# Optimization experiments

Hardware: AMD Instinct MI355X
Metric: run time of the kernel (lower is better)

## Reference

```python
import jax, jax.numpy as jnp
import numpy as np

DIM = 1024
NUM_HEADS = 16
HEAD_DIM = DIM // NUM_HEADS
SCALE = HEAD_DIM ** -0.5


def setup_inputs() -> dict:
    key = jax.random.key(0)
    ks = jax.random.split(key, 6)
    B, N = 2, 2048
    s = DIM ** -0.5
    return {
        "x": jax.random.normal(ks[0], (B, N, DIM), dtype=jnp.float32),
        "Wq": jax.random.normal(ks[1], (DIM, DIM), dtype=jnp.float32) * s,
        "Wk": jax.random.normal(ks[2], (DIM, DIM), dtype=jnp.float32) * s,
        "Wv": jax.random.normal(ks[3], (DIM, DIM), dtype=jnp.float32) * s,
        "Wp": jax.random.normal(ks[4], (DIM, DIM), dtype=jnp.float32) * s,
        "bp": jax.random.normal(ks[5], (DIM,), dtype=jnp.float32) * 0.01,
    }


def reference(x, Wq, Wk, Wv, Wp, bp):
    B, N, C = x.shape
    H, D = NUM_HEADS, HEAD_DIM
    # projections (torch Linear: x @ W.T); reshape to (B, H, N, D)
    q = (x @ Wq.T).reshape(B, N, H, D).transpose(0, 2, 1, 3)
    k = (x @ Wk.T).reshape(B, N, H, D).transpose(0, 2, 1, 3)
    v = (x @ Wv.T).reshape(B, N, H, D).transpose(0, 2, 1, 3)
    attn = jnp.einsum("bhnd,bhmd->bhnm", q, k) * SCALE
    attn = jax.nn.softmax(attn, axis=-1)  # dropout p=0 -> identity
    out = jnp.einsum("bhnm,bhmd->bhnd", attn, v)
    out = out.transpose(0, 2, 1, 3).reshape(B, N, C)
    return out @ Wp.T + bp
```

## Files before the change

### kernel.cpp

```cpp
#include <hip/hip_runtime.h>
#include <cstdint>

#define DIMC   1024
#define NHEADS 16
#define HD     64
#define BATCH  2
#define SEQ    2048
#define MROWS  (BATCH*SEQ)
#define QSCALE2 0.18033688f

typedef __bf16 bf16x8 __attribute__((ext_vector_type(8)));
typedef float  f32x4  __attribute__((ext_vector_type(4)));

#define AST 88
#define TST 136

__device__ __forceinline__ unsigned short f2bf(float f) {
    union { float f; unsigned int u; } v; v.f = f;
    unsigned int u = v.u;
    u += 0x7fffu + ((u >> 16) & 1u);
    return (unsigned short)(u >> 16);
}

__device__ __forceinline__ unsigned int pk2bf(float a, float b) {
    union { float f; unsigned int u; } ua, ub;
    ua.f = a; ub.f = b;
    return __builtin_amdgcn_perm(ub.u + 0x8000u, ua.u + 0x8000u, 0x07060302u);
}

__device__ __forceinline__ void gload_lds16(const void* g, void* l) {
    __builtin_amdgcn_global_load_lds(
        (const __attribute__((address_space(1))) unsigned int*)g,
        (__attribute__((address_space(3))) unsigned int*)l, 16, 0, 0);
}

__global__ __launch_bounds__(256) void cast_all(
    const float* __restrict__ x,
    const float* __restrict__ Wq, const float* __restrict__ Wk,
    const float* __restrict__ Wv, const float* __restrict__ Wp,
    unsigned short* __restrict__ xb, unsigned short* __restrict__ Wb)
{
    const size_t M1 = (size_t)DIMC * DIMC;
    int y = blockIdx.y;
    const float* src;
    unsigned short* dst;
    if (y < 4)      { src = x  + (size_t)y * M1; dst = xb + (size_t)y * M1; }
    else if (y == 4){ src = Wq; dst = Wb; }
    else if (y == 5){ src = Wk; dst = Wb + M1; }
    else if (y == 6){ src = Wv; dst = Wb + 2 * M1; }
    else            { src = Wp; dst = Wb + 3 * M1; }
    size_t idx = ((size_t)blockIdx.x * 256 + threadIdx.x) * 4;
    float4 v = *(const float4*)(src + idx);
    ushort4 p; p.x = f2bf(v.x); p.y = f2bf(v.y); p.z = f2bf(v.z); p.w = f2bf(v.w);
    *(ushort4*)(dst + idx) = p;
}

__device__ __forceinline__ void gemm_issue(
    const unsigned short* __restrict__ A, const unsigned short* __restrict__ B,
    unsigned short* As, unsigned short* Bs, int m0, int n0, int kt)
{
    const int t = threadIdx.x;
    const int w = t >> 6, lane = t & 63;
    const int srow = lane >> 3, scol = lane & 7;
#pragma unroll
    for (int i = 0; i < 4; ++i) {
        int r  = i * 32 + w * 8 + srow;
        int cg = scol ^ (r & 7);
        gload_lds16(A + (size_t)(m0 + r) * DIMC + kt + cg * 8, As + r * 64 + scol * 8);
        gload_lds16(B + (size_t)(n0 + r) * DIMC + kt + cg * 8, Bs + r * 64 + scol * 8);
    }
}

__device__ __forceinline__ void gemm_compute(
    const unsigned short* As, const unsigned short* Bs, f32x4 acc[4][4])
{
    const int t = threadIdx.x;
    const int w = t >> 6, lane = t & 63, quad = lane >> 4, lr = lane & 15;
    const int wr = w >> 1, wc = w & 1;
#pragma unroll
    for (int kk = 0; kk < 2; ++kk) {
        bf16x8 af[4], bfr[4];
#pragma unroll
        for (int mt = 0; mt < 4; ++mt) {
            int row = wr * 64 + mt * 16 + lr;
            int cb  = kk * 4 + quad;
            af[mt] = *(const bf16x8*)&As[row * 64 + (cb ^ (row & 7)) * 8];
        }
#pragma unroll
        for (int nt = 0; nt < 4; ++nt) {
            int row = wc * 64 + nt * 16 + lr;
            int cb  = kk * 4 + quad;
            bfr[nt] = *(const bf16x8*)&Bs[row * 64 + (cb ^ (row & 7)) * 8];
        }
#pragma unroll
        for (int mt = 0; mt < 4; ++mt)
#pragma unroll
            for (int nt = 0; nt < 4; ++nt)
                acc[mt][nt] = __builtin_amdgcn_mfma_f32_16x16x32_bf16(af[mt], bfr[nt], acc[mt][nt], 0, 0, 0);
    }
}

__device__ __forceinline__ void gemm_k_loop_db(
    const unsigned short* __restrict__ A, const unsigned short* __restrict__ B,
    unsigned short* smem, int m0, int n0, f32x4 acc[4][4])
{
    unsigned short* As0 = smem;
    unsigned short* Bs0 = smem + 8192;
    unsigned short* As1 = smem + 16384;
    unsigned short* Bs1 = smem + 24576;

    gemm_issue(A, B, As0, Bs0, m0, n0, 0);
    for (int kt = 0; kt < DIMC; kt += 128) {
        __syncthreads();
        gemm_issue(A, B, As1, Bs1, m0, n0, kt + 64);
        gemm_compute(As0, Bs0, acc);
        __syncthreads();
        if (kt + 128 < DIMC) gemm_issue(A, B, As0, Bs0, m0, n0, kt + 128);
        gemm_compute(As1, Bs1, acc);
    }
}

__device__ __forceinline__ void vt_epilogue(
    unsigned short* Ts, f32x4 acc[4][4], int m0, int n0,
    unsigned short* __restrict__ vT)
{
    const int t = threadIdx.x;
    const int w = t >> 6, lane = t & 63, quad = lane >> 4, lr = lane & 15;
    const int wr = w >> 1, wc = w & 1;

    __syncthreads();
#pragma unroll
    for (int mt = 0; mt < 4; ++mt)
#pragma unroll
        for (int nt = 0; nt < 4; ++nt) {
            int lcol  = wc * 64 + nt * 16 + lr;
            int lrow0 = wr * 64 + mt * 16 + quad * 4;
            ushort4 p;
            p.x = f2bf(acc[mt][nt][0]); p.y = f2bf(acc[mt][nt][1]);
            p.z = f2bf(acc[mt][nt][2]); p.w = f2bf(acc[mt][nt][3]);
            *(ushort4*)&Ts[lcol * TST + lrow0] = p;
        }
    __syncthreads();

    int lc = t >> 1, half = t & 1;
    int cg = n0 + lc, hh = cg >> 6, dd = cg & 63;
    int bb = m0 >> 11, nn0 = m0 & (SEQ - 1);
    size_t dst = ((size_t)((bb * NHEADS + hh) * HD + dd)) * SEQ + nn0 + half * 64;
    const unsigned short* srcp = &Ts[lc * TST + half * 64];
#pragma unroll
    for (int i = 0; i < 8; ++i)
        *(uint4*)&vT[dst + i * 8] = *(const uint4*)&srcp[i * 8];
}

__global__ __launch_bounds__(256) void gemm_qkv_fast(
    const unsigned short* __restrict__ xb, const unsigned short* __restrict__ Wb,
    unsigned short* __restrict__ qo, unsigned short* __restrict__ ko,
    unsigned short* __restrict__ vT)
{
    __shared__ unsigned short smem[32768];

    const int t  = threadIdx.x;
    const int n0 = blockIdx.x * 128, m0 = blockIdx.y * 128, z = blockIdx.z;
    const unsigned short* B = Wb + (size_t)z * DIMC * DIMC;
    const int w = t >> 6, lane = t & 63, quad = lane >> 4, lr = lane & 15;
    const int wr = w >> 1, wc = w & 1;

    f32x4 acc[4][4];
#pragma unroll
    for (int mt = 0; mt < 4; ++mt)
#pragma unroll
        for (int nt = 0; nt < 4; ++nt)
#pragma unroll
            for (int r = 0; r < 4; ++r) acc[mt][nt][r] = 0.f;

    gemm_k_loop_db(xb, B, smem, m0, n0, acc);

    if (z == 2) {
        vt_epilogue(smem, acc, m0, n0, vT);
    } else {
        unsigned short* Out = (z == 0) ? qo : ko;
        const float sc = (z == 0) ? QSCALE2 : 1.0f;
#pragma unroll
        for (int mt = 0; mt < 4; ++mt)
#pragma unroll
            for (int nt = 0; nt < 4; ++nt)
#pragma unroll
                for (int r = 0; r < 4; ++r) {
                    int row = m0 + wr * 64 + mt * 16 + quad * 4 + r;
                    int col = n0 + wc * 64 + nt * 16 + lr;
                    Out[(size_t)row * DIMC + col] = f2bf(acc[mt][nt][r] * sc);
                }
    }
}

__global__ __launch_bounds__(256) void gemm_out_fast(
    const unsigned short* __restrict__ O, const unsigned short* __restrict__ Wpb,
    const float* __restrict__ bias, float* __restrict__ out)
{
    __shared__ unsigned short smem[32768];

    const int t  = threadIdx.x;
    const int n0 = blockIdx.x * 128, m0 = blockIdx.y * 128;
    const int w = t >> 6, lane = t & 63, quad = lane >> 4, lr = lane & 15;
    const int wr = w >> 1, wc = w & 1;

    f32x4 acc[4][4];
#pragma unroll
    for (int mt = 0; mt < 4; ++mt)
#pragma unroll
        for (int nt = 0; nt < 4; ++nt)
#pragma unroll
            for (int r = 0; r < 4; ++r) acc[mt][nt][r] = 0.f;

    gemm_k_loop_db(O, Wpb, smem, m0, n0, acc);

#pragma unroll
    for (int mt = 0; mt < 4; ++mt)
#pragma unroll
        for (int nt = 0; nt < 4; ++nt)
#pragma unroll
            for (int r = 0; r < 4; ++r) {
                int row = m0 + wr * 64 + mt * 16 + quad * 4 + r;
                int col = n0 + wc * 64 + nt * 16 + lr;
                out[(size_t)row * DIMC + col] = acc[mt][nt][r] + bias[col];
            }
}

__global__ __launch_bounds__(256) void attn_kernel(
    const unsigned short* __restrict__ qg, const unsigned short* __restrict__ kg,
    const unsigned short* __restrict__ vT, unsigned short* __restrict__ og)
{
    __shared__ unsigned short Ka[64 * 64];
    __shared__ unsigned short Kb[64 * 64];
    __shared__ unsigned short Va[64 * 64];
    __shared__ unsigned short Vb[64 * 64];
    __shared__ unsigned short Ps[128 * 64];

    const int t  = threadIdx.x;
    const int w = t >> 6, l = t & 63, quad = l >> 4, lr = l & 15;
    const int srow = t >> 3, scol = t & 7;
    const int pkey = (lr & 7) << 1;

    const int bid  = blockIdx.x;
    const int slot = bid >> 3;
    const int bh   = (bid & 7) * 4 + (slot >> 4);
    const int qt   = slot & 15;
    const int b    = bh >> 4, h = bh & 15;

    const unsigned short* khead = kg + ((size_t)(b * SEQ)) * DIMC + h * HD;
    const unsigned short* vhead = vT + (size_t)((b * NHEADS + h) * HD) * SEQ;

    bf16x8 qf[2][2];
#pragma unroll
    for (int mt = 0; mt < 2; ++mt) {
        const size_t qoff = ((size_t)(b * SEQ + qt * 128 + w * 32 + mt * 16 + lr)) * DIMC + h * HD;
        qf[mt][0] = *(const bf16x8*)(qg + qoff + 0  + quad * 8);
        qf[mt][1] = *(const bf16x8*)(qg + qoff + 32 + quad * 8);
    }

    bf16x8 ones;
#pragma unroll
    for (int j = 0; j < 8; ++j) ones[j] = (__bf16)1.0f;
    const f32x4 fzero = { 0.f, 0.f, 0.f, 0.f };

    f32x4 o_acc[2][4], lacc[2];
#pragma unroll
    for (int mt = 0; mt < 2; ++mt) {
        lacc[mt] = fzero;
#pragma unroll
        for (int ct = 0; ct < 4; ++ct) o_acc[mt][ct] = fzero;
    }

    auto issue = [&](int kt, unsigned short* Kd, unsigned short* Vd) {
#pragma unroll
        for (int i = 0; i < 2; ++i) {
            int r  = i * 32 + srow;
            int cg = scol ^ (r & 7);
            gload_lds16(khead + (size_t)(kt * 64 + r) * DIMC + cg * 8, Kd + r * 64 + scol * 8);
            gload_lds16(vhead + (size_t)r * SEQ + kt * 64 + cg * 8,   Vd + r * 64 + scol * 8);
        }
    };

    auto compute = [&](const unsigned short* Kc, const unsigned short* Vc) {
        f32x4 s[2][4];
#pragma unroll
        for (int nt = 0; nt < 4; ++nt) {
            int row = nt * 16 + lr;
            bf16x8 kf = *(const bf16x8*)&Kc[row * 64 + ((quad ^ (row & 7)) * 8)];
#pragma unroll
            for (int mt = 0; mt < 2; ++mt)
                s[mt][nt] = __builtin_amdgcn_mfma_f32_16x16x32_bf16(kf, qf[mt][0], fzero, 0, 0, 0);
        }
#pragma unroll
        for (int nt = 0; nt < 4; ++nt) {
            int row = nt * 16 + lr;
            bf16x8 kf = *(const bf16x8*)&Kc[row * 64 + (((4 + quad) ^ (row & 7)) * 8)];
#pragma unroll
            for (int mt = 0; mt < 2; ++mt)
                s[mt][nt] = __builtin_amdgcn_mfma_f32_16x16x32_bf16(kf, qf[mt][1], s[mt][nt], 0, 0, 0);
        }

#pragma unroll
        for (int mt = 0; mt < 2; ++mt)
#pragma unroll
            for (int nt = 0; nt < 4; ++nt) {
                uint2 pp;
                pp.x = pk2bf(__builtin_amdgcn_exp2f(s[mt][nt][0]),
                             __builtin_amdgcn_exp2f(s[mt][nt][1]));
                pp.y = pk2bf(__builtin_amdgcn_exp2f(s[mt][nt][2]),
                             __builtin_amdgcn_exp2f(s[mt][nt][3]));
                *(uint2*)&Ps[(w * 32 + mt * 16 + lr) * 64 + (((nt * 4 + quad) ^ pkey) * 4)] = pp;
            }

#pragma unroll
        for (int kk = 0; kk < 2; ++kk) {
            bf16x8 vf[4];
#pragma unroll
            for (int ct = 0; ct < 4; ++ct) {
                int row = ct * 16 + lr;
                vf[ct] = *(const bf16x8*)&Vc[row * 64 + (((kk * 4 + quad) ^ (row & 7)) * 8)];
            }
#pragma unroll
            for (int mt = 0; mt < 2; ++mt) {
                bf16x8 pf = *(const bf16x8*)&Ps[(w * 32 + mt * 16 + lr) * 64 + (((kk * 8 + quad * 2) ^ pkey) * 4)];
                lacc[mt] = __builtin_amdgcn_mfma_f32_16x16x32_bf16(pf, ones, lacc[mt], 0, 0, 0);
#pragma unroll
                for (int ct = 0; ct < 4; ++ct)
                    o_acc[mt][ct] = __builtin_amdgcn_mfma_f32_16x16x32_bf16(pf, vf[ct], o_acc[mt][ct], 0, 0, 0);
            }
        }
    };

    issue(0, Ka, Va);
    for (int kt = 0; kt < SEQ / 64; kt += 2) {
        __syncthreads();
        issue(kt + 1, Kb, Vb);
        compute(Ka, Va);

        __syncthreads();
        if (kt + 2 < SEQ / 64) issue(kt + 2, Ka, Va);
        compute(Kb, Vb);
    }

#pragma unroll
    for (int mt = 0; mt < 2; ++mt) {
        float inv[4];
#pragma unroll
        for (int r = 0; r < 4; ++r) inv[r] = 1.0f / lacc[mt][r];
#pragma unroll
        for (int ct = 0; ct < 4; ++ct)
#pragma unroll
            for (int r = 0; r < 4; ++r) {
                int qrow = qt * 128 + w * 32 + mt * 16 + quad * 4 + r;
                og[((size_t)(b * SEQ + qrow)) * DIMC + h * HD + ct * 16 + lr] =
                    f2bf(o_acc[mt][ct][r] * inv[r]);
            }
    }
}

__global__ __launch_bounds__(256) void gemm_qkv_f32(
    const float* __restrict__ x,
    const float* __restrict__ Wq, const float* __restrict__ Wk, const float* __restrict__ Wv,
    unsigned short* __restrict__ qo, unsigned short* __restrict__ ko, unsigned short* __restrict__ vT)
{
    __shared__ unsigned short smem[2 * 128 * AST];
    unsigned short* As = smem;
    unsigned short* Bs = smem + 128 * AST;

    const int t  = threadIdx.x;
    const int n0 = blockIdx.x * 128, m0 = blockIdx.y * 128, z = blockIdx.z;
    const float* W = (z == 0) ? Wq : (z == 1) ? Wk : Wv;
    const int w = t >> 6, l = t & 63, quad = l >> 4, lr = l & 15;
    const int wr = w >> 1, wc = w & 1;

    f32x4 acc[4][4];
#pragma unroll
    for (int mt = 0; mt < 4; ++mt)
#pragma unroll
        for (int nt = 0; nt < 4; ++nt)
#pragma unroll
            for (int r = 0; r < 4; ++r) acc[mt][nt][r] = 0.f;

    for (int kt = 0; kt < DIMC; kt += 64) {
        __syncthreads();
#pragma unroll
        for (int i = 0; i < 8; ++i) {
            int flat = t + i * 256;
            int row = flat >> 4, seg = flat & 15;
            float4 a = *(const float4*)(x + (size_t)(m0 + row) * DIMC + kt + seg * 4);
            ushort4 pa; pa.x = f2bf(a.x); pa.y = f2bf(a.y); pa.z = f2bf(a.z); pa.w = f2bf(a.w);
            *(ushort4*)&As[row * AST + seg * 4] = pa;
            float4 b = *(const float4*)(W + (size_t)(n0 + row) * DIMC + kt + seg * 4);
            ushort4 pb; pb.x = f2bf(b.x); pb.y = f2bf(b.y); pb.z = f2bf(b.z); pb.w = f2bf(b.w);
            *(ushort4*)&Bs[row * AST + seg * 4] = pb;
        }
        __syncthreads();
#pragma unroll
        for (int kk = 0; kk < 2; ++kk) {
            bf16x8 af[4], bfr[4];
#pragma unroll
            for (int mt = 0; mt < 4; ++mt)
                af[mt] = *(const bf16x8*)&As[(wr * 64 + mt * 16 + lr) * AST + kk * 32 + quad * 8];
#pragma unroll
            for (int nt = 0; nt < 4; ++nt)
                bfr[nt] = *(const bf16x8*)&Bs[(wc * 64 + nt * 16 + lr) * AST + kk * 32 + quad * 8];
#pragma unroll
            for (int mt = 0; mt < 4; ++mt)
#pragma unroll
                for (int nt = 0; nt < 4; ++nt)
                    acc[mt][nt] = __builtin_amdgcn_mfma_f32_16x16x32_bf16(af[mt], bfr[nt], acc[mt][nt], 0, 0, 0);
        }
    }

    if (z == 2) {
        __syncthreads();
#pragma unroll
        for (int mt = 0; mt < 4; ++mt)
#pragma unroll
            for (int nt = 0; nt < 4; ++nt) {
                int lcol  = wc * 64 + nt * 16 + lr;
                int lrow0 = wr * 64 + mt * 16 + quad * 4;
                ushort4 p;
                p.x = f2bf(acc[mt][nt][0]); p.y = f2bf(acc[mt][nt][1]);
                p.z = f2bf(acc[mt][nt][2]); p.w = f2bf(acc[mt][nt][3]);
                *(ushort4*)&smem[lcol * TST + lrow0] = p;
            }
        __syncthreads();
        int lc = t >> 1, half = t & 1;
        int cg = n0 + lc, hh = cg >> 6, dd = cg & 63;
        int bb = m0 >> 11, nn0 = m0 & (SEQ - 1);
        size_t dst = ((size_t)((bb * NHEADS + hh) * HD + dd)) * SEQ + nn0 + half * 64;
        const unsigned short* srcp = &smem[lc * TST + half * 64];
#pragma unroll
        for (int i = 0; i < 8; ++i)
            *(uint4*)&vT[dst + i * 8] = *(const uint4*)&srcp[i * 8];
    } else {
        unsigned short* Out = (z == 0) ? qo : ko;
        const float sc = (z == 0) ? QSCALE2 : 1.0f;
#pragma unroll
        for (int mt = 0; mt < 4; ++mt)
#pragma unroll
            for (int nt = 0; nt < 4; ++nt)
#pragma unroll
                for (int r = 0; r < 4; ++r) {
                    int row = m0 + wr * 64 + mt * 16 + quad * 4 + r;
                    int col = n0 + wc * 64 + nt * 16 + lr;
                    Out[(size_t)row * DIMC + col] = f2bf(acc[mt][nt][r] * sc);
                }
    }
}

__global__ __launch_bounds__(256) void gemm_out_f32(
    const unsigned short* __restrict__ A, const float* __restrict__ Wp,
    const float* __restrict__ bias, float* __restrict__ out)
{
    __shared__ unsigned short As[128 * AST];
    __shared__ unsigned short Bs[128 * AST];

    const int t  = threadIdx.x;
    const int n0 = blockIdx.x * 128, m0 = blockIdx.y * 128;
    const int w = t >> 6, l = t & 63, quad = l >> 4, lr = l & 15;
    const int wr = w >> 1, wc = w & 1;

    f32x4 acc[4][4];
#pragma unroll
    for (int mt = 0; mt < 4; ++mt)
#pragma unroll
        for (int nt = 0; nt < 4; ++nt)
#pragma unroll
            for (int r = 0; r < 4; ++r) acc[mt][nt][r] = 0.f;

    for (int kt = 0; kt < DIMC; kt += 64) {
        __syncthreads();
#pragma unroll
        for (int i = 0; i < 8; ++i) {
            int flat = t + i * 256;
            int row = flat >> 4, seg = flat & 15;
            ushort4 a = *(const ushort4*)(A + (size_t)(m0 + row) * DIMC + kt + seg * 4);
            *(ushort4*)&As[row * AST + seg * 4] = a;
            float4 b = *(const float4*)(Wp + (size_t)(n0 + row) * DIMC + kt + seg * 4);
            ushort4 pb; pb.x = f2bf(b.x); pb.y = f2bf(b.y); pb.z = f2bf(b.z); pb.w = f2bf(b.w);
            *(ushort4*)&Bs[row * AST + seg * 4] = pb;
        }
        __syncthreads();
#pragma unroll
        for (int kk = 0; kk < 2; ++kk) {
            bf16x8 af[4], bfr[4];
#pragma unroll
            for (int mt = 0; mt < 4; ++mt)
                af[mt] = *(const bf16x8*)&As[(wr * 64 + mt * 16 + lr) * AST + kk * 32 + quad * 8];
#pragma unroll
            for (int nt = 0; nt < 4; ++nt)
                bfr[nt] = *(const bf16x8*)&Bs[(wc * 64 + nt * 16 + lr) * AST + kk * 32 + quad * 8];
#pragma unroll
            for (int mt = 0; mt < 4; ++mt)
#pragma unroll
                for (int nt = 0; nt < 4; ++nt)
                    acc[mt][nt] = __builtin_amdgcn_mfma_f32_16x16x32_bf16(af[mt], bfr[nt], acc[mt][nt], 0, 0, 0);
        }
    }

#pragma unroll
    for (int mt = 0; mt < 4; ++mt)
#pragma unroll
        for (int nt = 0; nt < 4; ++nt)
#pragma unroll
            for (int r = 0; r < 4; ++r) {
                int row = m0 + wr * 64 + mt * 16 + quad * 4 + r;
                int col = n0 + wc * 64 + nt * 16 + lr;
                out[(size_t)row * DIMC + col] = acc[mt][nt][r] + bias[col];
            }
}

extern "C" void kernel_launch(void* const* d_in, const int* in_sizes, int n_in,
                              void* d_out, int out_size, void* d_ws, size_t ws_size,
                              hipStream_t stream)
{
    const float* x  = (const float*)d_in[0];
    const float* Wq = (const float*)d_in[1];
    const float* Wk = (const float*)d_in[2];
    const float* Wv = (const float*)d_in[3];
    const float* Wp = (const float*)d_in[4];
    const float* bp = (const float*)d_in[5];
    float* out = (float*)d_out;

    const size_t SZ  = (size_t)MROWS * DIMC;
    const size_t WSZ = (size_t)DIMC * DIMC;
    const size_t need = (4 * SZ + 4 * WSZ) * sizeof(unsigned short);

    if (ws_size >= need) {
        unsigned short* q  = (unsigned short*)d_ws;
        unsigned short* k  = q + SZ;
        unsigned short* vt = k + SZ;
        unsigned short* o  = vt + SZ;
        unsigned short* Wb = o + SZ;
        unsigned short* xb = (unsigned short*)d_out;

        cast_all<<<dim3(1024, 8), 256, 0, stream>>>(x, Wq, Wk, Wv, Wp, xb, Wb);
        gemm_qkv_fast<<<dim3(DIMC / 128, MROWS / 128, 3), 256, 0, stream>>>(xb, Wb, q, k, vt);
        attn_kernel<<<dim3(512), 256, 0, stream>>>(q, k, vt, o);
        gemm_out_fast<<<dim3(DIMC / 128, MROWS / 128), 256, 0, stream>>>(o, Wb + 3 * WSZ, bp, out);
    } else {
        unsigned short* q  = (unsigned short*)d_ws;
        unsigned short* k  = q + SZ;
        unsigned short* vt = k + SZ;
        unsigned short* o  = vt + SZ;

        gemm_qkv_f32<<<dim3(DIMC / 128, MROWS / 128, 3), 256, 0, stream>>>(x, Wq, Wk, Wv, q, k, vt);
        attn_kernel<<<dim3(512), 256, 0, stream>>>(q, k, vt, o);
        gemm_out_f32<<<dim3(DIMC / 128, MROWS / 128), 256, 0, stream>>>(o, Wp, bp, out);
    }
}
```

Measured before the change: 179.8 us.

## Split attention over key halves with combine pass; shrink GEMM K-tile to 32

Attention is split into two halves along the key sequence. This doubles the block count from 512 to 1024 to improve occupancy on the many-CU device. Each half writes fp32 partial outputs and row sums, and a new combine kernel merges them into bf16. The QKV and output GEMMs now use a 32-wide K tile, which halves LDS use per block so more blocks can be resident. The V-transpose epilogue gets an XOR-swizzled LDS layout. The costs are extra fp32 traffic for the partial results, one more kernel launch, and more barriers in the GEMM loop.

```diff
diff --git a/kernel.cpp b/kernel.cpp
--- a/kernel.cpp
+++ b/kernel.cpp
@@ -55,72 +55,66 @@
     *(ushort4*)(dst + idx) = p;
 }
 
-__device__ __forceinline__ void gemm_issue(
+__device__ __forceinline__ void gemm_issue32(
     const unsigned short* __restrict__ A, const unsigned short* __restrict__ B,
     unsigned short* As, unsigned short* Bs, int m0, int n0, int kt)
 {
     const int t = threadIdx.x;
-    const int w = t >> 6, lane = t & 63;
-    const int srow = lane >> 3, scol = lane & 7;
-#pragma unroll
-    for (int i = 0; i < 4; ++i) {
-        int r  = i * 32 + w * 8 + srow;
-        int cg = scol ^ (r & 7);
-        gload_lds16(A + (size_t)(m0 + r) * DIMC + kt + cg * 8, As + r * 64 + scol * 8);
-        gload_lds16(B + (size_t)(n0 + r) * DIMC + kt + cg * 8, Bs + r * 64 + scol * 8);
-    }
-}
-
-__device__ __forceinline__ void gemm_compute(
+    const int srow = t >> 2, scol = t & 3;
+#pragma unroll
+    for (int i = 0; i < 2; ++i) {
+        int r  = i * 64 + srow;
+        int cg = scol ^ (r & 3);
+        gload_lds16(A + (size_t)(m0 + r) * DIMC + kt + cg * 8, As + r * 32 + scol * 8);
+        gload_lds16(B + (size_t)(n0 + r) * DIMC + kt + cg * 8, Bs + r * 32 + scol * 8);
+    }
+}
+
+__device__ __forceinline__ void gemm_compute32(
     const unsigned short* As, const unsigned short* Bs, f32x4 acc[4][4])
 {
     const int t = threadIdx.x;
     const int w = t >> 6, lane = t & 63, quad = lane >> 4, lr = lane & 15;
     const int wr = w >> 1, wc = w & 1;
-#pragma unroll
-    for (int kk = 0; kk < 2; ++kk) {
-        bf16x8 af[4], bfr[4];
-#pragma unroll
-        for (int mt = 0; mt < 4; ++mt) {
-            int row = wr * 64 + mt * 16 + lr;
-            int cb  = kk * 4 + quad;
-            af[mt] = *(const bf16x8*)&As[row * 64 + (cb ^ (row & 7)) * 8];
-        }
-#pragma unroll
-        for (int nt = 0; nt < 4; ++nt) {
-            int row = wc * 64 + nt * 16 + lr;
-            int cb  = kk * 4 + quad;
-            bfr[nt] = *(const bf16x8*)&Bs[row * 64 + (cb ^ (row & 7)) * 8];
-        }
-#pragma unroll
-        for (int mt = 0; mt < 4; ++mt)
-#pragma unroll
-            for (int nt = 0; nt < 4; ++nt)
-                acc[mt][nt] = __builtin_amdgcn_mfma_f32_16x16x32_bf16(af[mt], bfr[nt], acc[mt][nt], 0, 0, 0);
-    }
-}
-
-__device__ __forceinline__ void gemm_k_loop_db(
+    bf16x8 af[4], bfr[4];
+#pragma unroll
+    for (int mt = 0; mt < 4; ++mt) {
+        int row = wr * 64 + mt * 16 + lr;
+        af[mt] = *(const bf16x8*)&As[row * 32 + ((quad ^ (row & 3)) * 8)];
+    }
+#pragma unroll
+    for (int nt = 0; nt < 4; ++nt) {
+        int row = wc * 64 + nt * 16 + lr;
+        bfr[nt] = *(const bf16x8*)&Bs[row * 32 + ((quad ^ (row & 3)) * 8)];
+    }
+#pragma unroll
+    for (int mt = 0; mt < 4; ++mt)
+#pragma unroll
+        for (int nt = 0; nt < 4; ++nt)
+            acc[mt][nt] = __builtin_amdgcn_mfma_f32_16x16x32_bf16(af[mt], bfr[nt], acc[mt][nt], 0, 0, 0);
+}
+
+__device__ __forceinline__ void gemm_k_loop32(
     const unsigned short* __restrict__ A, const unsigned short* __restrict__ B,
     unsigned short* smem, int m0, int n0, f32x4 acc[4][4])
 {
     unsigned short* As0 = smem;
-    unsigned short* Bs0 = smem + 8192;
-    unsigned short* As1 = smem + 16384;
-    unsigned short* Bs1 = smem + 24576;
-
-    gemm_issue(A, B, As0, Bs0, m0, n0, 0);
-    for (int kt = 0; kt < DIMC; kt += 128) {
-        __syncthreads();
-        gemm_issue(A, B, As1, Bs1, m0, n0, kt + 64);
-        gemm_compute(As0, Bs0, acc);
-        __syncthreads();
-        if (kt + 128 < DIMC) gemm_issue(A, B, As0, Bs0, m0, n0, kt + 128);
-        gemm_compute(As1, Bs1, acc);
-    }
-}
-
-__device__ __forceinline__ void vt_epilogue(
+    unsigned short* Bs0 = smem + 4096;
+    unsigned short* As1 = smem + 8192;
+    unsigned short* Bs1 = smem + 12288;
+
+    gemm_issue32(A, B, As0, Bs0, m0, n0, 0);
+    for (int kt = 0; kt < DIMC; kt += 64) {
+        __syncthreads();
+        gemm_issue32(A, B, As1, Bs1, m0, n0, kt + 32);
+        gemm_compute32(As0, Bs0, acc);
+        __syncthreads();
+        if (kt + 64 < DIMC) gemm_issue32(A, B, As0, Bs0, m0, n0, kt + 64);
+        gemm_compute32(As1, Bs1, acc);
+    }
+}
+
+__device__ __forceinline__ void vt_epilogue32(
     unsigned short* Ts, f32x4 acc[4][4], int m0, int n0,
     unsigned short* __restrict__ vT)
 {
@@ -135,10 +129,11 @@
         for (int nt = 0; nt < 4; ++nt) {
             int lcol  = wc * 64 + nt * 16 + lr;
             int lrow0 = wr * 64 + mt * 16 + quad * 4;
+            int c = (lrow0 >> 3) ^ (lcol & 7);
             ushort4 p;
             p.x = f2bf(acc[mt][nt][0]); p.y = f2bf(acc[mt][nt][1]);
             p.z = f2bf(acc[mt][nt][2]); p.w = f2bf(acc[mt][nt][3]);
-            *(ushort4*)&Ts[lcol * TST + lrow0] = p;
+            *(ushort4*)&Ts[lcol * 128 + c * 8 + (lrow0 & 7)] = p;
         }
     __syncthreads();
 
@@ -146,10 +141,11 @@
     int cg = n0 + lc, hh = cg >> 6, dd = cg & 63;
     int bb = m0 >> 11, nn0 = m0 & (SEQ - 1);
     size_t dst = ((size_t)((bb * NHEADS + hh) * HD + dd)) * SEQ + nn0 + half * 64;
-    const unsigned short* srcp = &Ts[lc * TST + half * 64];
-#pragma unroll
-    for (int i = 0; i < 8; ++i)
-        *(uint4*)&vT[dst + i * 8] = *(const uint4*)&srcp[i * 8];
+#pragma unroll
+    for (int i = 0; i < 8; ++i) {
+        int c = (half * 8 + i) ^ (lc & 7);
+        *(uint4*)&vT[dst + i * 8] = *(const uint4*)&Ts[lc * 128 + c * 8];
+    }
 }
 
 __global__ __launch_bounds__(256) void gemm_qkv_fast(
@@ -157,7 +153,7 @@
     unsigned short* __restrict__ qo, unsigned short* __restrict__ ko,
     unsigned short* __restrict__ vT)
 {
-    __shared__ unsigned short smem[32768];
+    __shared__ unsigned short smem[16384];
 
     const int t  = threadIdx.x;
     const int n0 = blockIdx.x * 128, m0 = blockIdx.y * 128, z = blockIdx.z;
@@ -173,10 +169,10 @@
 #pragma unroll
             for (int r = 0; r < 4; ++r) acc[mt][nt][r] = 0.f;
 
-    gemm_k_loop_db(xb, B, smem, m0, n0, acc);
+    gemm_k_loop32(xb, B, smem, m0, n0, acc);
 
     if (z == 2) {
-        vt_epilogue(smem, acc, m0, n0, vT);
+        vt_epilogue32(smem, acc, m0, n0, vT);
     } else {
         unsigned short* Out = (z == 0) ? qo : ko;
         const float sc = (z == 0) ? QSCALE2 : 1.0f;
@@ -197,7 +193,7 @@
     const unsigned short* __restrict__ O, const unsigned short* __restrict__ Wpb,
     const float* __restrict__ bias, float* __restrict__ out)
 {
-    __shared__ unsigned short smem[32768];
+    __shared__ unsigned short smem[16384];
 
     const int t  = threadIdx.x;
     const int n0 = blockIdx.x * 128, m0 = blockIdx.y * 128;
@@ -212,7 +208,7 @@
 #pragma unroll
             for (int r = 0; r < 4; ++r) acc[mt][nt][r] = 0.f;
 
-    gemm_k_loop_db(O, Wpb, smem, m0, n0, acc);
+    gemm_k_loop32(O, Wpb, smem, m0, n0, acc);
 
 #pragma unroll
     for (int mt = 0; mt < 4; ++mt)
@@ -336,7 +332,6 @@
         __syncthreads();
         issue(kt + 1, Kb, Vb);
         compute(Ka, Va);
-
         __syncthreads();
         if (kt + 2 < SEQ / 64) issue(kt + 2, Ka, Va);
         compute(Kb, Vb);
@@ -356,6 +351,166 @@
                     f2bf(o_acc[mt][ct][r] * inv[r]);
             }
     }
+}
+
+__global__ __launch_bounds__(256) void attn_split(
+    const unsigned short* __restrict__ qg, const unsigned short* __restrict__ kg,
+    const unsigned short* __restrict__ vT,
+    float* __restrict__ Opart, float* __restrict__ Lpart)
+{
+    __shared__ unsigned short Ka[64 * 64];
+    __shared__ unsigned short Kb[64 * 64];
+    __shared__ unsigned short Va[64 * 64];
+    __shared__ unsigned short Vb[64 * 64];
+    __shared__ unsigned short Ps[128 * 64];
+
+    const int t  = threadIdx.x;
+    const int w = t >> 6, l = t & 63, quad = l >> 4, lr = l & 15;
+    const int srow = t >> 3, scol = t & 7;
+    const int pkey = (lr & 7) << 1;
+
+    const int bid  = blockIdx.x;
+    const int slot = bid >> 3;
+    const int bh   = (bid & 7) * 4 + (slot >> 5);
+    const int rem  = slot & 31;
+    const int qt   = rem >> 1;
+    const int hk   = rem & 1;
+    const int b    = bh >> 4, h = bh & 15;
+    const int kts  = hk * (SEQ / 128);
+
+    float* Op = Opart + (size_t)hk * MROWS * DIMC;
+    float* Lp = Lpart + (size_t)hk * MROWS * NHEADS;
+
+    const unsigned short* khead = kg + ((size_t)(b * SEQ)) * DIMC + h * HD;
+    const unsigned short* vhead = vT + (size_t)((b * NHEADS + h) * HD) * SEQ;
+
+    bf16x8 qf[2][2];
+#pragma unroll
+    for (int mt = 0; mt < 2; ++mt) {
+        const size_t qoff = ((size_t)(b * SEQ + qt * 128 + w * 32 + mt * 16 + lr)) * DIMC + h * HD;
+        qf[mt][0] = *(const bf16x8*)(qg + qoff + 0  + quad * 8);
+        qf[mt][1] = *(const bf16x8*)(qg + qoff + 32 + quad * 8);
+    }
+
+    bf16x8 ones;
+#pragma unroll
+    for (int j = 0; j < 8; ++j) ones[j] = (__bf16)1.0f;
+    const f32x4 fzero = { 0.f, 0.f, 0.f, 0.f };
+
+    f32x4 o_acc[2][4], lacc[2];
+#pragma unroll
+    for (int mt = 0; mt < 2; ++mt) {
+        lacc[mt] = fzero;
+#pragma unroll
+        for (int ct = 0; ct < 4; ++ct) o_acc[mt][ct] = fzero;
+    }
+
+    auto issue = [&](int kt, unsigned short* Kd, unsigned short* Vd) {
+#pragma unroll
+        for (int i = 0; i < 2; ++i) {
+            int r  = i * 32 + srow;
+            int cg = scol ^ (r & 7);
+            gload_lds16(khead + (size_t)(kt * 64 + r) * DIMC + cg * 8, Kd + r * 64 + scol * 8);
+            gload_lds16(vhead + (size_t)r * SEQ + kt * 64 + cg * 8,   Vd + r * 64 + scol * 8);
+        }
+    };
+
+    auto compute = [&](const unsigned short* Kc, const unsigned short* Vc) {
+        f32x4 s[2][4];
+#pragma unroll
+        for (int nt = 0; nt < 4; ++nt) {
+            int row = nt * 16 + lr;
+            bf16x8 kf = *(const bf16x8*)&Kc[row * 64 + ((quad ^ (row & 7)) * 8)];
+#pragma unroll
+            for (int mt = 0; mt < 2; ++mt)
+                s[mt][nt] = __builtin_amdgcn_mfma_f32_16x16x32_bf16(kf, qf[mt][0], fzero, 0, 0, 0);
+        }
+#pragma unroll
+        for (int nt = 0; nt < 4; ++nt) {
+            int row = nt * 16 + lr;
+            bf16x8 kf = *(const bf16x8*)&Kc[row * 64 + (((4 + quad) ^ (row & 7)) * 8)];
+#pragma unroll
+            for (int mt = 0; mt < 2; ++mt)
+                s[mt][nt] = __builtin_amdgcn_mfma_f32_16x16x32_bf16(kf, qf[mt][1], s[mt][nt], 0, 0, 0);
+        }
+
+#pragma unroll
+        for (int mt = 0; mt < 2; ++mt)
+#pragma unroll
+            for (int nt = 0; nt < 4; ++nt) {
+                uint2 pp;
+                pp.x = pk2bf(__builtin_amdgcn_exp2f(s[mt][nt][0]),
+                             __builtin_amdgcn_exp2f(s[mt][nt][1]));
+                pp.y = pk2bf(__builtin_amdgcn_exp2f(s[mt][nt][2]),
+                             __builtin_amdgcn_exp2f(s[mt][nt][3]));
+                *(uint2*)&Ps[(w * 32 + mt * 16 + lr) * 64 + (((nt * 4 + quad) ^ pkey) * 4)] = pp;
+            }
+
+#pragma unroll
+        for (int kk = 0; kk < 2; ++kk) {
+            bf16x8 vf[4];
+#pragma unroll
+            for (int ct = 0; ct < 4; ++ct) {
+                int row = ct * 16 + lr;
+                vf[ct] = *(const bf16x8*)&Vc[row * 64 + (((kk * 4 + quad) ^ (row & 7)) * 8)];
+            }
+#pragma unroll
+            for (int mt = 0; mt < 2; ++mt) {
+                bf16x8 pf = *(const bf16x8*)&Ps[(w * 32 + mt * 16 + lr) * 64 + (((kk * 8 + quad * 2) ^ pkey) * 4)];
+                lacc[mt] = __builtin_amdgcn_mfma_f32_16x16x32_bf16(pf, ones, lacc[mt], 0, 0, 0);
+#pragma unroll
+                for (int ct = 0; ct < 4; ++ct)
+                    o_acc[mt][ct] = __builtin_amdgcn_mfma_f32_16x16x32_bf16(pf, vf[ct], o_acc[mt][ct], 0, 0, 0);
+            }
+        }
+    };
+
+    issue(kts, Ka, Va);
+    for (int kt = 0; kt < SEQ / 128; kt += 2) {
+        __syncthreads();
+        issue(kts + kt + 1, Kb, Vb);
+        compute(Ka, Va);
+        __syncthreads();
+        if (kt + 2 < SEQ / 128) issue(kts + kt + 2, Ka, Va);
+        compute(Kb, Vb);
+    }
+
+#pragma unroll
+    for (int mt = 0; mt < 2; ++mt) {
+#pragma unroll
+        for (int ct = 0; ct < 4; ++ct)
+#pragma unroll
+            for (int r = 0; r < 4; ++r) {
+                int qrow = qt * 128 + w * 32 + mt * 16 + quad * 4 + r;
+                Op[((size_t)(b * SEQ + qrow)) * DIMC + h * HD + ct * 16 + lr] = o_acc[mt][ct][r];
+            }
+        if (lr == 0) {
+#pragma unroll
+            for (int r = 0; r < 4; ++r) {
+                int qrow = qt * 128 + w * 32 + mt * 16 + quad * 4 + r;
+                Lp[(size_t)(b * SEQ + qrow) * NHEADS + h] = lacc[mt][r];
+            }
+        }
+    }
+}
+
+__global__ __launch_bounds__(256) void combine_kernel(
+    const float* __restrict__ O0, const float* __restrict__ O1,
+    const float* __restrict__ L0, const float* __restrict__ L1,
+    unsigned short* __restrict__ o)
+{
+    size_t i4 = (size_t)blockIdx.x * 256 + threadIdx.x;
+    size_t i  = i4 * 4;
+    int m = (int)(i >> 10);
+    int h = (int)((i >> 6) & 15);
+    size_t r = (size_t)m * NHEADS + h;
+    float inv = 1.0f / (L0[r] + L1[r]);
+    float4 a = *(const float4*)(O0 + i);
+    float4 bb = *(const float4*)(O1 + i);
+    ushort4 p;
+    p.x = f2bf((a.x + bb.x) * inv); p.y = f2bf((a.y + bb.y) * inv);
+    p.z = f2bf((a.z + bb.z) * inv); p.w = f2bf((a.w + bb.w) * inv);
+    *(ushort4*)(o + i) = p;
 }
 
 __global__ __launch_bounds__(256) void gemm_qkv_f32(
@@ -526,9 +681,11 @@
 
     const size_t SZ  = (size_t)MROWS * DIMC;
     const size_t WSZ = (size_t)DIMC * DIMC;
-    const size_t need = (4 * SZ + 4 * WSZ) * sizeof(unsigned short);
-
-    if (ws_size >= need) {
+    const size_t LSZ = (size_t)MROWS * NHEADS;
+    const size_t need1 = (4 * SZ + 4 * WSZ) * sizeof(unsigned short);
+    const size_t need2 = need1 + 2 * SZ * sizeof(float) + 2 * LSZ * sizeof(float);
+
+    if (ws_size >= need1) {
         unsigned short* q  = (unsigned short*)d_ws;
         unsigned short* k  = q + SZ;
         unsigned short* vt = k + SZ;
@@ -538,7 +695,15 @@
 
         cast_all<<<dim3(1024, 8), 256, 0, stream>>>(x, Wq, Wk, Wv, Wp, xb, Wb);
         gemm_qkv_fast<<<dim3(DIMC / 128, MROWS / 128, 3), 256, 0, stream>>>(xb, Wb, q, k, vt);
-        attn_kernel<<<dim3(512), 256, 0, stream>>>(q, k, vt, o);
+
+        if (ws_size >= need2) {
+            float* Op = (float*)(Wb + 4 * WSZ);
+            float* Lp = Op + 2 * SZ;
+            attn_split<<<dim3(1024), 256, 0, stream>>>(q, k, vt, Op, Lp);
+            combine_kernel<<<dim3(SZ / 1024), 256, 0, stream>>>(Op, Op + SZ, Lp, Lp + LSZ, o);
+        } else {
+            attn_kernel<<<dim3(512), 256, 0, stream>>>(q, k, vt, o);
+        }
         gemm_out_fast<<<dim3(DIMC / 128, MROWS / 128), 256, 0, stream>>>(o, Wb + 3 * WSZ, bp, out);
     } else {
         unsigned short* q  = (unsigned short*)d_ws;
```

Result: slower. 203.4 us (+13.1%).
